# Optimization experiments

Hardware: AMD Instinct MI355X
Metric: run time of the kernel (lower is better)

## Reference

```python
import jax, jax.numpy as jnp
import numpy as np

BSZ, DIM, SEQ_A, SEQ_B = 16, 768, 1024, 1024


def setup_inputs() -> dict:
    key = jax.random.key(0)
    kA, kB, kU = jax.random.split(key, 3)
    input_A = jax.random.normal(kA, (BSZ, DIM, SEQ_A), dtype=jnp.float32)
    input_B = jax.random.normal(kB, (BSZ, DIM, SEQ_B), dtype=jnp.float32)
    intput_msk = jnp.zeros((BSZ, SEQ_A, SEQ_B), dtype=jnp.float32)  # 0 = on, -inf = off
    U = jax.random.normal(kU, (DIM, DIM), dtype=jnp.float32)
    return {"input_A": input_A, "input_B": input_B, "intput_msk": intput_msk, "U": U}


def reference(input_A, input_B, intput_msk, U):
    # align[b,s,t] = tanh( A[b,:,s]^T U B[b,:,t] )  -> (bsz, seq_A, seq_B)
    align = jnp.einsum("bds,de,bet->bst", input_A, U, input_B)
    align = jnp.tanh(align) + intput_msk
    # per-token scores: max over the other modality's sequence, then softmax
    score_A = jax.nn.softmax(jnp.max(align, axis=2), axis=-1)  # (bsz, seq_A)
    score_B = jax.nn.softmax(jnp.max(align, axis=1), axis=-1)  # (bsz, seq_B)
    output_A = jnp.einsum("bds,bs->bd", input_A, score_A)  # (bsz, dim_A)
    output_B = jnp.einsum("bdt,bt->bd", input_B, score_B)  # (bsz, dim_B)
    return (output_A, output_B)
```

## Files before the change

### kernel.cpp

```cpp
#include <hip/hip_runtime.h>
#include <math.h>

#define BSZ  16
#define DIM  768
#define SEQA 1024
#define SEQB 1024

typedef float f32x4 __attribute__((ext_vector_type(4)));
typedef long long llong;

__device__ inline void gload_lds16(const void* g, void* l) {
    __builtin_amdgcn_global_load_lds(
        (const __attribute__((address_space(1))) void*)g,
        (__attribute__((address_space(3))) void*)l, 16, 0, 0);
}

__device__ inline unsigned enc_key(float f) {
    unsigned u = __float_as_uint(f);
    return (u & 0x80000000u) ? ~u : (u | 0x80000000u);
}
__device__ inline float dec_key(unsigned k) {
    return (k & 0x80000000u) ? __uint_as_float(k ^ 0x80000000u) : __uint_as_float(~k);
}

__device__ inline unsigned pk4_fp8(float a, float b, float c, float d) {
    int v = 0;
    v = __builtin_amdgcn_cvt_pk_fp8_f32(a, b, v, false);
    v = __builtin_amdgcn_cvt_pk_fp8_f32(c, d, v, true);
    return (unsigned)v;
}
__device__ inline unsigned char f2fp8(float a) {
    return (unsigned char)(__builtin_amdgcn_cvt_pk_fp8_f32(a, a, 0, false) & 0xFF);
}

__device__ inline float fast_tanh(float x) {
    float ax = fabsf(x);
    float u = __expf(-2.0f * ax);
    float th = __fdividef(1.0f - u, 1.0f + u);
    return copysignf(th, x);
}

__global__ __launch_bounds__(256) void t_cast_AB(const float* __restrict__ A,
                                                 const float* __restrict__ B,
                                                 unsigned char* __restrict__ At,
                                                 unsigned char* __restrict__ Bt) {
    __shared__ float tl[64][68];
    const int z = blockIdx.z;
    const float* X = (z < BSZ) ? A : B;
    unsigned char* Y = (z < BSZ) ? At : Bt;
    const int b = z & 15;
    const int d0 = blockIdx.y * 64;
    const int s0 = blockIdx.x * 64;
    const int tid = threadIdx.x;
    const int rr = tid >> 4, c4 = tid & 15;
    const float* Xb = X + ((size_t)b * DIM + d0) * SEQA + s0;
#pragma unroll
    for (int i = 0; i < 4; i++) {
        int row = i * 16 + rr;
        float4 v = *(const float4*)&Xb[(size_t)row * SEQA + c4 * 4];
        *(float4*)&tl[row][c4 * 4] = v;
    }
    __syncthreads();
    unsigned char* Yb = Y + ((size_t)b * SEQA + s0) * DIM + d0;
    const int m = tid & 15, sl = tid >> 4;
#pragma unroll
    for (int i = 0; i < 4; i++) {
        int s = sl + 16 * i;
        unsigned v = pk4_fp8(tl[4 * m + 0][s], tl[4 * m + 1][s], tl[4 * m + 2][s], tl[4 * m + 3][s]);
        *(unsigned*)&Yb[(size_t)s * DIM + 4 * m] = v;
    }
}

__global__ __launch_bounds__(256) void t_cast_U(const float* __restrict__ U,
                                                unsigned char* __restrict__ Ut,
                                                unsigned* __restrict__ keyA,
                                                unsigned* __restrict__ keyB) {
    __shared__ float tl[64][68];
    const int d0 = blockIdx.y * 64;
    const int e0 = blockIdx.x * 64;
    const int tid = threadIdx.x;
    const int bid = blockIdx.y * gridDim.x + blockIdx.x;
    if (bid < 64) {
        int i = bid * 256 + tid;
        keyA[i] = 0u;
        keyB[i] = 0u;
    }
    const int rr = tid >> 4, c4 = tid & 15;
#pragma unroll
    for (int i = 0; i < 4; i++) {
        int row = i * 16 + rr;
        float4 v = *(const float4*)&U[(size_t)(d0 + row) * DIM + e0 + c4 * 4];
        *(float4*)&tl[row][c4 * 4] = v;
    }
    __syncthreads();
    const int m = tid & 15, sl = tid >> 4;
#pragma unroll
    for (int i = 0; i < 4; i++) {
        int e = sl + 16 * i;
        unsigned v = pk4_fp8(tl[4 * m + 0][e], tl[4 * m + 1][e], tl[4 * m + 2][e], tl[4 * m + 3][e]);
        *(unsigned*)&Ut[(size_t)(e0 + e) * DIM + d0 + 4 * m] = v;
    }
}

__device__ inline void stage_tile(const unsigned char* __restrict__ src, int row0,
                                  int kbyte0, unsigned char* lds, int wid, int lane) {
    const int r8 = lane >> 3;
    const int g  = lane & 7;
    const int gg = g ^ (r8 & 7);
#pragma unroll
    for (int t = 0; t < 4; ++t) {
        int row = row0 + wid * 32 + t * 8 + r8;
        gload_lds16(src + (size_t)row * DIM + kbyte0 + gg * 16,
                    lds + (wid * 32 + t * 8) * 128 + lane * 16);
    }
}

__device__ inline llong frag_read(const unsigned char* lds, int rowbase, int l15,
                                  int quad, int h) {
    int gg = 2 * h + (quad >> 1);
    int off = (rowbase + l15) * 128 + ((gg ^ (l15 & 7)) << 4) + (quad & 1) * 8;
    return *(const llong*)(lds + off);
}

#define TB (256 * 128)

__device__ __forceinline__ void ktile_mfma(const unsigned char* Ms, const unsigned char* Ns,
                                           int wr, int wc, int l15, int quad,
                                           f32x4 (&acc)[8][4]) {
#pragma unroll
    for (int h = 0; h < 4; ++h) {
        llong av[8], bv[4];
#pragma unroll
        for (int i = 0; i < 8; ++i) av[i] = frag_read(Ms, wr * 128 + 16 * i, l15, quad, h);
#pragma unroll
        for (int j = 0; j < 4; ++j) bv[j] = frag_read(Ns, wc * 64 + 16 * j, l15, quad, h);
#pragma unroll
        for (int i = 0; i < 8; ++i)
#pragma unroll
            for (int j = 0; j < 4; ++j)
                acc[i][j] = __builtin_amdgcn_mfma_f32_16x16x32_fp8_fp8(av[i], bv[j], acc[i][j], 0, 0, 0);
    }
}

#define KLOOP(MSRC, NSRC, MS, NS)                                                   \
    stage_tile(MSRC, 0, 0, MS, wid, lane);                                          \
    stage_tile(NSRC, 0, 0, NS, wid, lane);                                          \
    stage_tile(MSRC, 0, 128, MS + TB, wid, lane);                                   \
    stage_tile(NSRC, 0, 128, NS + TB, wid, lane);                                   \
    _Pragma("unroll")                                                               \
    for (int kt = 0; kt < DIM / 128; ++kt) {                                        \
        if (kt < DIM / 128 - 1) asm volatile("s_waitcnt vmcnt(8)" ::: "memory");    \
        else                    asm volatile("s_waitcnt vmcnt(0)" ::: "memory");    \
        __builtin_amdgcn_s_barrier();                                               \
        asm volatile("" ::: "memory");                                              \
        __builtin_amdgcn_s_setprio(1);                                              \
        ktile_mfma(MS + (kt & 1) * TB, NS + (kt & 1) * TB, wr, wc, l15, quad, acc); \
        __builtin_amdgcn_s_setprio(0);                                              \
        asm volatile("s_waitcnt lgkmcnt(0)" ::: "memory");                          \
        __builtin_amdgcn_s_barrier();                                               \
        asm volatile("" ::: "memory");                                              \
        if (kt + 2 < DIM / 128) {                                                   \
            stage_tile(MSRC, 0, (kt + 2) * 128, MS + (kt & 1) * TB, wid, lane);     \
            stage_tile(NSRC, 0, (kt + 2) * 128, NS + (kt & 1) * TB, wid, lane);     \
        }                                                                           \
    }

__global__ __launch_bounds__(512, 2) void k1_ua(const unsigned char* __restrict__ At,
                                                const unsigned char* __restrict__ Ut,
                                                unsigned char* __restrict__ Ct) {
    __shared__ __align__(16) unsigned char As[2 * TB];
    __shared__ __align__(16) unsigned char Us[2 * TB];
    const int b  = blockIdx.z;
    const int s0 = blockIdx.x * 256;
    const int e0 = blockIdx.y * 256;
    const int tid = threadIdx.x;
    const int lane = tid & 63;
    const int wid = tid >> 6;
    const int wr = wid >> 2, wc = wid & 3;
    const int quad = lane >> 4, l15 = lane & 15;

    const unsigned char* Atb = At + ((size_t)b * SEQA + s0) * DIM;
    const unsigned char* Utb = Ut + (size_t)e0 * DIM;

    f32x4 acc[8][4] = {};

    KLOOP(Atb, Utb, As, Us)

    unsigned char* Cb = Ct + (size_t)b * SEQA * DIM;
#pragma unroll
    for (int i = 0; i < 8; ++i)
#pragma unroll
        for (int j = 0; j < 4; ++j) {
            int e_g = e0 + wc * 64 + 16 * j + l15;
#pragma unroll
            for (int r = 0; r < 4; ++r) {
                int s_g = s0 + wr * 128 + 16 * i + quad * 4 + r;
                Cb[(size_t)s_g * DIM + e_g] = f2fp8(acc[i][j][r]);
            }
        }
}

__global__ __launch_bounds__(512, 2) void k2_align(const unsigned char* __restrict__ Ct,
                                                   const unsigned char* __restrict__ Bt,
                                                   const float* __restrict__ msk,
                                                   unsigned* __restrict__ keyA,
                                                   unsigned* __restrict__ keyB) {
    __shared__ __align__(16) unsigned char Cs[2 * TB];
    __shared__ __align__(16) unsigned char Bs[2 * TB];
    const int b  = blockIdx.z;
    const int t0 = blockIdx.x * 256;
    const int s0 = blockIdx.y * 256;
    const int tid = threadIdx.x;
    const int lane = tid & 63;
    const int wid = tid >> 6;
    const int wr = wid >> 2, wc = wid & 3;
    const int quad = lane >> 4, l15 = lane & 15;

    const unsigned char* Btb = Bt + ((size_t)b * SEQB + t0) * DIM;
    const unsigned char* Ctb = Ct + ((size_t)b * SEQA + s0) * DIM;

    f32x4 acc[8][4] = {};

    KLOOP(Btb, Ctb, Bs, Cs)

    const float* Mb = msk + (size_t)b * SEQA * SEQB;
#pragma unroll
    for (int i = 0; i < 8; ++i)
#pragma unroll
        for (int j = 0; j < 4; ++j) {
            int s_g = s0 + wc * 64 + 16 * j + l15;
            int t_g = t0 + wr * 128 + 16 * i + quad * 4;
            float4 mvv = *(const float4*)&Mb[(size_t)s_g * SEQB + t_g];
            acc[i][j][0] = fast_tanh(acc[i][j][0]) + mvv.x;
            acc[i][j][1] = fast_tanh(acc[i][j][1]) + mvv.y;
            acc[i][j][2] = fast_tanh(acc[i][j][2]) + mvv.z;
            acc[i][j][3] = fast_tanh(acc[i][j][3]) + mvv.w;
        }
#pragma unroll
    for (int j = 0; j < 4; ++j) {
        float m = -INFINITY;
#pragma unroll
        for (int i = 0; i < 8; ++i)
#pragma unroll
            for (int r = 0; r < 4; ++r) m = fmaxf(m, acc[i][j][r]);
        m = fmaxf(m, __shfl_xor(m, 16));
        m = fmaxf(m, __shfl_xor(m, 32));
        if (quad == 0)
            atomicMax(&keyA[b * SEQA + s0 + wc * 64 + 16 * j + l15], enc_key(m));
    }
#pragma unroll
    for (int i = 0; i < 8; ++i)
#pragma unroll
        for (int r = 0; r < 4; ++r) {
            float m = fmaxf(fmaxf(acc[i][0][r], acc[i][1][r]), fmaxf(acc[i][2][r], acc[i][3][r]));
            m = fmaxf(m, __shfl_xor(m, 1));
            m = fmaxf(m, __shfl_xor(m, 2));
            m = fmaxf(m, __shfl_xor(m, 4));
            m = fmaxf(m, __shfl_xor(m, 8));
            if (l15 == 0)
                atomicMax(&keyB[b * SEQB + t0 + wr * 128 + 16 * i + quad * 4 + r], enc_key(m));
        }
}

__global__ __launch_bounds__(256) void k3_softmax(const unsigned* __restrict__ keyA,
                                                  const unsigned* __restrict__ keyB,
                                                  float* __restrict__ scoreA,
                                                  float* __restrict__ scoreB) {
    const int b = blockIdx.x;
    const bool isA = (blockIdx.y == 0);
    const unsigned* keys = isA ? (keyA + b * SEQA) : (keyB + b * SEQB);
    float* score = isA ? (scoreA + b * SEQA) : (scoreB + b * SEQB);
    __shared__ float sh[4];
    const int tid = threadIdx.x;
    float m[4];
    float mx = -INFINITY;
#pragma unroll
    for (int k = 0; k < 4; k++) {
        m[k] = dec_key(keys[tid + 256 * k]);
        mx = fmaxf(mx, m[k]);
    }
#pragma unroll
    for (int o = 32; o > 0; o >>= 1) mx = fmaxf(mx, __shfl_down(mx, o, 64));
    if ((tid & 63) == 0) sh[tid >> 6] = mx;
    __syncthreads();
    mx = fmaxf(fmaxf(sh[0], sh[1]), fmaxf(sh[2], sh[3]));
    __syncthreads();
    float e[4];
    float sum = 0.f;
#pragma unroll
    for (int k = 0; k < 4; k++) { e[k] = expf(m[k] - mx); sum += e[k]; }
#pragma unroll
    for (int o = 32; o > 0; o >>= 1) sum += __shfl_down(sum, o, 64);
    if ((tid & 63) == 0) sh[tid >> 6] = sum;
    __syncthreads();
    sum = sh[0] + sh[1] + sh[2] + sh[3];
    float inv = 1.0f / sum;
#pragma unroll
    for (int k = 0; k < 4; k++) score[tid + 256 * k] = e[k] * inv;
}

__global__ __launch_bounds__(256) void k4_out(const float* __restrict__ A,
                                              const float* __restrict__ B,
                                              const float* __restrict__ scoreA,
                                              const float* __restrict__ scoreB,
                                              float* __restrict__ out) {
    const int which = blockIdx.y;
    const int row = blockIdx.x * 4 + (threadIdx.x >> 6);
    const int lane = threadIdx.x & 63;
    const float* X = which ? B : A;
    const float* S = which ? scoreB : scoreA;
    const int b = row / DIM;
    const float4* xr = (const float4*)(X + (size_t)row * SEQA);
    const float4* sr = (const float4*)(S + (size_t)b * SEQA);
    float acc = 0.f;
#pragma unroll
    for (int q = lane; q < SEQA / 4; q += 64) {
        float4 x = xr[q];
        float4 s = sr[q];
        acc += x.x * s.x + x.y * s.y + x.z * s.z + x.w * s.w;
    }
#pragma unroll
    for (int o = 32; o > 0; o >>= 1) acc += __shfl_down(acc, o, 64);
    if (lane == 0) out[which * (BSZ * DIM) + row] = acc;
}

extern "C" void kernel_launch(void* const* d_in, const int* in_sizes, int n_in,
                              void* d_out, int out_size, void* d_ws, size_t ws_size,
                              hipStream_t stream) {
    const float* A   = (const float*)d_in[0];
    const float* B   = (const float*)d_in[1];
    const float* msk = (const float*)d_in[2];
    const float* U   = (const float*)d_in[3];
    float* out = (float*)d_out;

    char* ws = (char*)d_ws;
    unsigned char* At = (unsigned char*)ws;
    unsigned char* Bt = (unsigned char*)(ws + 12582912);
    unsigned char* Ct = (unsigned char*)(ws + 25165824);
    unsigned char* Ut = (unsigned char*)(ws + 37748736);
    unsigned* keyA   = (unsigned*)(ws + 38338560);
    unsigned* keyB   = (unsigned*)(ws + 38404096);
    float*    scoreA = (float*)   (ws + 38469632);
    float*    scoreB = (float*)   (ws + 38535168);

    t_cast_U<<<dim3(DIM / 64, DIM / 64, 1), 256, 0, stream>>>(U, Ut, keyA, keyB);
    t_cast_AB<<<dim3(SEQA / 64, DIM / 64, 2 * BSZ), 256, 0, stream>>>(A, B, At, Bt);
    k1_ua<<<dim3(SEQA / 256, DIM / 256, BSZ), 512, 0, stream>>>(At, Ut, Ct);
    k2_align<<<dim3(SEQB / 256, SEQA / 256, BSZ), 512, 0, stream>>>(Ct, Bt, msk, keyA, keyB);
    k3_softmax<<<dim3(BSZ, 2), 256, 0, stream>>>(keyA, keyB, scoreA, scoreB);
    k4_out<<<dim3(BSZ * DIM / 4, 2), 256, 0, stream>>>(A, B, scoreA, scoreB, out);
}
```

Baseline: 255.0 us.

## Shrink GEMM tiles to 128x128 with 256 threads and drop double buffering

Both FP8 GEMM kernels (U·A projection and the alignment GEMM) move from 256x256 tiles with 8 waves and a double-buffered LDS pipeline to 128x128 tiles with 4 waves and a simple single-buffered loop. The aim is to launch four times as many blocks, so the grid fills all CUs rather than leaving many idle, and to cut LDS use so more blocks fit per CU. In exchange, global loads no longer overlap with MFMA work, each tile gets less operand reuse, and there are two full barriers per k-step. The mask loads in the epilogue are also batched per column group.

```diff
diff --git a/kernel.cpp b/kernel.cpp
--- a/kernel.cpp
+++ b/kernel.cpp
@@ -122,125 +122,117 @@
     return *(const llong*)(lds + off);
 }
 
-#define TB (256 * 128)
-
-__device__ __forceinline__ void ktile_mfma(const unsigned char* Ms, const unsigned char* Ns,
-                                           int wr, int wc, int l15, int quad,
-                                           f32x4 (&acc)[8][4]) {
-#pragma unroll
-    for (int h = 0; h < 4; ++h) {
-        llong av[8], bv[4];
-#pragma unroll
-        for (int i = 0; i < 8; ++i) av[i] = frag_read(Ms, wr * 128 + 16 * i, l15, quad, h);
-#pragma unroll
-        for (int j = 0; j < 4; ++j) bv[j] = frag_read(Ns, wc * 64 + 16 * j, l15, quad, h);
-#pragma unroll
-        for (int i = 0; i < 8; ++i)
-#pragma unroll
-            for (int j = 0; j < 4; ++j)
-                acc[i][j] = __builtin_amdgcn_mfma_f32_16x16x32_fp8_fp8(av[i], bv[j], acc[i][j], 0, 0, 0);
-    }
-}
-
-#define KLOOP(MSRC, NSRC, MS, NS)                                                   \
-    stage_tile(MSRC, 0, 0, MS, wid, lane);                                          \
-    stage_tile(NSRC, 0, 0, NS, wid, lane);                                          \
-    stage_tile(MSRC, 0, 128, MS + TB, wid, lane);                                   \
-    stage_tile(NSRC, 0, 128, NS + TB, wid, lane);                                   \
-    _Pragma("unroll")                                                               \
-    for (int kt = 0; kt < DIM / 128; ++kt) {                                        \
-        if (kt < DIM / 128 - 1) asm volatile("s_waitcnt vmcnt(8)" ::: "memory");    \
-        else                    asm volatile("s_waitcnt vmcnt(0)" ::: "memory");    \
-        __builtin_amdgcn_s_barrier();                                               \
-        asm volatile("" ::: "memory");                                              \
-        __builtin_amdgcn_s_setprio(1);                                              \
-        ktile_mfma(MS + (kt & 1) * TB, NS + (kt & 1) * TB, wr, wc, l15, quad, acc); \
-        __builtin_amdgcn_s_setprio(0);                                              \
-        asm volatile("s_waitcnt lgkmcnt(0)" ::: "memory");                          \
-        __builtin_amdgcn_s_barrier();                                               \
-        asm volatile("" ::: "memory");                                              \
-        if (kt + 2 < DIM / 128) {                                                   \
-            stage_tile(MSRC, 0, (kt + 2) * 128, MS + (kt & 1) * TB, wid, lane);     \
-            stage_tile(NSRC, 0, (kt + 2) * 128, NS + (kt & 1) * TB, wid, lane);     \
-        }                                                                           \
-    }
-
-__global__ __launch_bounds__(512, 2) void k1_ua(const unsigned char* __restrict__ At,
+__global__ __launch_bounds__(256, 3) void k1_ua(const unsigned char* __restrict__ At,
                                                 const unsigned char* __restrict__ Ut,
                                                 unsigned char* __restrict__ Ct) {
-    __shared__ __align__(16) unsigned char As[2 * TB];
-    __shared__ __align__(16) unsigned char Us[2 * TB];
+    __shared__ __align__(16) unsigned char As[128 * 128];
+    __shared__ __align__(16) unsigned char Us[128 * 128];
     const int b  = blockIdx.z;
-    const int s0 = blockIdx.x * 256;
-    const int e0 = blockIdx.y * 256;
+    const int s0 = blockIdx.x * 128;
+    const int e0 = blockIdx.y * 128;
     const int tid = threadIdx.x;
     const int lane = tid & 63;
     const int wid = tid >> 6;
-    const int wr = wid >> 2, wc = wid & 3;
+    const int wr = wid >> 1, wc = wid & 1;
     const int quad = lane >> 4, l15 = lane & 15;
 
-    const unsigned char* Atb = At + ((size_t)b * SEQA + s0) * DIM;
-    const unsigned char* Utb = Ut + (size_t)e0 * DIM;
-
-    f32x4 acc[8][4] = {};
-
-    KLOOP(Atb, Utb, As, Us)
-
+    const unsigned char* Atb = At + (size_t)b * SEQA * DIM;
+    f32x4 acc[4][4] = {};
+
+    for (int d0 = 0; d0 < DIM; d0 += 128) {
+        stage_tile(Atb + (size_t)s0 * DIM, 0, d0, As, wid, lane);
+        stage_tile(Ut + (size_t)e0 * DIM, 0, d0, Us, wid, lane);
+        __syncthreads();
+#pragma unroll
+        for (int h = 0; h < 4; ++h) {
+            llong av[4], bv[4];
+#pragma unroll
+            for (int i = 0; i < 4; ++i) av[i] = frag_read(As, wr * 64 + 16 * i, l15, quad, h);
+#pragma unroll
+            for (int j = 0; j < 4; ++j) bv[j] = frag_read(Us, wc * 64 + 16 * j, l15, quad, h);
+#pragma unroll
+            for (int i = 0; i < 4; ++i)
+#pragma unroll
+                for (int j = 0; j < 4; ++j)
+                    acc[i][j] = __builtin_amdgcn_mfma_f32_16x16x32_fp8_fp8(av[i], bv[j], acc[i][j], 0, 0, 0);
+        }
+        __syncthreads();
+    }
     unsigned char* Cb = Ct + (size_t)b * SEQA * DIM;
 #pragma unroll
-    for (int i = 0; i < 8; ++i)
+    for (int i = 0; i < 4; ++i)
 #pragma unroll
         for (int j = 0; j < 4; ++j) {
             int e_g = e0 + wc * 64 + 16 * j + l15;
 #pragma unroll
             for (int r = 0; r < 4; ++r) {
-                int s_g = s0 + wr * 128 + 16 * i + quad * 4 + r;
+                int s_g = s0 + wr * 64 + 16 * i + quad * 4 + r;
                 Cb[(size_t)s_g * DIM + e_g] = f2fp8(acc[i][j][r]);
             }
         }
 }
 
-__global__ __launch_bounds__(512, 2) void k2_align(const unsigned char* __restrict__ Ct,
+__global__ __launch_bounds__(256, 3) void k2_align(const unsigned char* __restrict__ Ct,
                                                    const unsigned char* __restrict__ Bt,
                                                    const float* __restrict__ msk,
                                                    unsigned* __restrict__ keyA,
                                                    unsigned* __restrict__ keyB) {
-    __shared__ __align__(16) unsigned char Cs[2 * TB];
-    __shared__ __align__(16) unsigned char Bs[2 * TB];
+    __shared__ __align__(16) unsigned char Cs[128 * 128];
+    __shared__ __align__(16) unsigned char Bs[128 * 128];
     const int b  = blockIdx.z;
-    const int t0 = blockIdx.x * 256;
-    const int s0 = blockIdx.y * 256;
+    const int t0 = blockIdx.x * 128;
+    const int s0 = blockIdx.y * 128;
     const int tid = threadIdx.x;
     const int lane = tid & 63;
     const int wid = tid >> 6;
-    const int wr = wid >> 2, wc = wid & 3;
+    const int wr = wid >> 1, wc = wid & 1;
     const int quad = lane >> 4, l15 = lane & 15;
 
-    const unsigned char* Btb = Bt + ((size_t)b * SEQB + t0) * DIM;
-    const unsigned char* Ctb = Ct + ((size_t)b * SEQA + s0) * DIM;
-
-    f32x4 acc[8][4] = {};
-
-    KLOOP(Btb, Ctb, Bs, Cs)
+    f32x4 acc[4][4] = {};
+
+    for (int e0 = 0; e0 < DIM; e0 += 128) {
+        stage_tile(Ct + (size_t)(b * SEQA + s0) * DIM, 0, e0, Cs, wid, lane);
+        stage_tile(Bt + (size_t)(b * SEQB + t0) * DIM, 0, e0, Bs, wid, lane);
+        __syncthreads();
+#pragma unroll
+        for (int h = 0; h < 4; ++h) {
+            llong av[4], bv[4];
+#pragma unroll
+            for (int i = 0; i < 4; ++i) av[i] = frag_read(Bs, wr * 64 + 16 * i, l15, quad, h);
+#pragma unroll
+            for (int j = 0; j < 4; ++j) bv[j] = frag_read(Cs, wc * 64 + 16 * j, l15, quad, h);
+#pragma unroll
+            for (int i = 0; i < 4; ++i)
+#pragma unroll
+                for (int j = 0; j < 4; ++j)
+                    acc[i][j] = __builtin_amdgcn_mfma_f32_16x16x32_fp8_fp8(av[i], bv[j], acc[i][j], 0, 0, 0);
+        }
+        __syncthreads();
+    }
 
     const float* Mb = msk + (size_t)b * SEQA * SEQB;
 #pragma unroll
-    for (int i = 0; i < 8; ++i)
-#pragma unroll
-        for (int j = 0; j < 4; ++j) {
-            int s_g = s0 + wc * 64 + 16 * j + l15;
-            int t_g = t0 + wr * 128 + 16 * i + quad * 4;
-            float4 mvv = *(const float4*)&Mb[(size_t)s_g * SEQB + t_g];
-            acc[i][j][0] = fast_tanh(acc[i][j][0]) + mvv.x;
-            acc[i][j][1] = fast_tanh(acc[i][j][1]) + mvv.y;
-            acc[i][j][2] = fast_tanh(acc[i][j][2]) + mvv.z;
-            acc[i][j][3] = fast_tanh(acc[i][j][3]) + mvv.w;
-        }
+    for (int j = 0; j < 4; ++j) {
+        int s_g = s0 + wc * 64 + 16 * j + l15;
+        float4 mvv[4];
+#pragma unroll
+        for (int i = 0; i < 4; ++i) {
+            int t_g = t0 + wr * 64 + 16 * i + quad * 4;
+            mvv[i] = *(const float4*)&Mb[(size_t)s_g * SEQB + t_g];
+        }
+#pragma unroll
+        for (int i = 0; i < 4; ++i) {
+            acc[i][j][0] = fast_tanh(acc[i][j][0]) + mvv[i].x;
+            acc[i][j][1] = fast_tanh(acc[i][j][1]) + mvv[i].y;
+            acc[i][j][2] = fast_tanh(acc[i][j][2]) + mvv[i].z;
+            acc[i][j][3] = fast_tanh(acc[i][j][3]) + mvv[i].w;
+        }
+    }
 #pragma unroll
     for (int j = 0; j < 4; ++j) {
         float m = -INFINITY;
 #pragma unroll
-        for (int i = 0; i < 8; ++i)
+        for (int i = 0; i < 4; ++i)
 #pragma unroll
             for (int r = 0; r < 4; ++r) m = fmaxf(m, acc[i][j][r]);
         m = fmaxf(m, __shfl_xor(m, 16));
@@ -249,7 +241,7 @@
             atomicMax(&keyA[b * SEQA + s0 + wc * 64 + 16 * j + l15], enc_key(m));
     }
 #pragma unroll
-    for (int i = 0; i < 8; ++i)
+    for (int i = 0; i < 4; ++i)
 #pragma unroll
         for (int r = 0; r < 4; ++r) {
             float m = fmaxf(fmaxf(acc[i][0][r], acc[i][1][r]), fmaxf(acc[i][2][r], acc[i][3][r]));
@@ -258,7 +250,7 @@
             m = fmaxf(m, __shfl_xor(m, 4));
             m = fmaxf(m, __shfl_xor(m, 8));
             if (l15 == 0)
-                atomicMax(&keyB[b * SEQB + t0 + wr * 128 + 16 * i + quad * 4 + r], enc_key(m));
+                atomicMax(&keyB[b * SEQB + t0 + wr * 64 + 16 * i + quad * 4 + r], enc_key(m));
         }
 }
 
@@ -345,8 +337,8 @@
 
     t_cast_U<<<dim3(DIM / 64, DIM / 64, 1), 256, 0, stream>>>(U, Ut, keyA, keyB);
     t_cast_AB<<<dim3(SEQA / 64, DIM / 64, 2 * BSZ), 256, 0, stream>>>(A, B, At, Bt);
-    k1_ua<<<dim3(SEQA / 256, DIM / 256, BSZ), 512, 0, stream>>>(At, Ut, Ct);
-    k2_align<<<dim3(SEQB / 256, SEQA / 256, BSZ), 512, 0, stream>>>(Ct, Bt, msk, keyA, keyB);
+    k1_ua<<<dim3(SEQA / 128, DIM / 128, BSZ), 256, 0, stream>>>(At, Ut, Ct);
+    k2_align<<<dim3(SEQB / 128, SEQA / 128, BSZ), 256, 0, stream>>>(Ct, Bt, msk, keyA, keyB);
     k3_softmax<<<dim3(BSZ, 2), 256, 0, stream>>>(keyA, keyB, scoreA, scoreB);
     k4_out<<<dim3(BSZ * DIM / 4, 2), 256, 0, stream>>>(A, B, scoreA, scoreB, out);
 }
```

Result: faster. 244.5 us (-4.1%).
